# Optimization experiments

Measured on AMD Instinct MI355X. Metric: run time of the kernel, lower is better.

Reference implementation:

```python
import jax, jax.numpy as jnp
import numpy as np
from jax import lax

B, T, D, H = 64, 512, 512, 512


def setup_inputs() -> dict:
    key = jax.random.key(0)
    k1, k2, k3, k4 = jax.random.split(key, 4)
    inputs = jax.random.normal(k1, (B, T, D), dtype=jnp.float32)
    lengths = jax.random.randint(k2, (B,), 1, T + 1, dtype=jnp.int32)
    c0 = jnp.zeros((B, H), dtype=jnp.float32)
    h0 = jnp.zeros((B, H), dtype=jnp.float32)
    scale_i = 1.0 / np.sqrt(D)
    scale_h = 1.0 / np.sqrt(H)
    Wi = jax.random.normal(k3, (D, 4 * H), dtype=jnp.float32) * scale_i
    Wh = jax.random.normal(k4, (H, 4 * H), dtype=jnp.float32) * scale_h
    b = jnp.zeros((4 * H,), dtype=jnp.float32)
    return {"inputs": inputs, "lengths": lengths, "c0": c0, "h0": h0,
            "Wi": Wi, "Wh": Wh, "b": b, "reverse": 1}


def _flip_sequences(seq, lengths):
    # seq: [B, T, F]; keeps padding at the end while flipping valid prefix.
    t = seq.shape[1]
    idxs = (jnp.arange(t - 1, -1, -1)[None, :] + lengths[:, None]) % t  # [B, T]
    return jnp.take_along_axis(seq, idxs[:, :, None], axis=1)


def reference(inputs, lengths, c0, h0, Wi, Wh, b, reverse):
    batch, t, _ = inputs.shape
    if reverse:
        inputs = _flip_sequences(inputs, lengths)

    def step(carry, x_t):
        c, h = carry
        z = x_t @ Wi + h @ Wh + b  # [B, 4H]
        i_g, f_g, g_g, o_g = jnp.split(z, 4, axis=-1)
        c_new = jax.nn.sigmoid(f_g) * c + jax.nn.sigmoid(i_g) * jnp.tanh(g_g)
        h_new = jax.nn.sigmoid(o_g) * jnp.tanh(c_new)
        return (c_new, h_new), (c_new, h_new)

    xs = jnp.swapaxes(inputs, 0, 1)  # [T, B, D]
    _, (cs, hs) = lax.scan(step, (c0, h0), xs)
    cs = jnp.swapaxes(cs, 0, 1)  # [B, T, H]
    hs = jnp.swapaxes(hs, 0, 1)  # [B, T, H]
    outputs = hs

    last = lengths - 1
    bidx = jnp.arange(batch)
    c_final = cs[bidx, last]
    h_final = hs[bidx, last]

    if reverse:
        outputs = _flip_sequences(outputs, lengths)
    return outputs, (c_final, h_final)
```

## Files before the change

### kernel.cpp

```cpp
#include <hip/hip_runtime.h>

#define B_ 64
#define T_ 512
#define D_ 512
#define H_ 512
#define NG 2048

typedef __attribute__((ext_vector_type(8))) short short8;
typedef __attribute__((ext_vector_type(4))) float floatx4;
typedef __attribute__((ext_vector_type(4))) unsigned int uintx4;

static __device__ __forceinline__ unsigned short f2bf(float f) {
    unsigned int u = __float_as_uint(f);
    return (unsigned short)((u + 0x7FFFu + ((u >> 16) & 1u)) >> 16);
}

static __device__ __forceinline__ short8 pack8(float4 a, float4 b) {
    short8 r;
    r[0] = (short)f2bf(a.x); r[1] = (short)f2bf(a.y);
    r[2] = (short)f2bf(a.z); r[3] = (short)f2bf(a.w);
    r[4] = (short)f2bf(b.x); r[5] = (short)f2bf(b.y);
    r[6] = (short)f2bf(b.z); r[7] = (short)f2bf(b.w);
    return r;
}

static __device__ __forceinline__ float sigm(float x) { return 1.0f / (1.0f + __expf(-x)); }
static __device__ __forceinline__ float tanh_(float x) {
    float e = __expf(2.0f * x);
    return 1.0f - 2.0f / (e + 1.0f);
}

__global__ __launch_bounds__(256) void transpose_w(
    const float* __restrict__ Wi, const float* __restrict__ Wh,
    unsigned short* __restrict__ WiT, unsigned short* __restrict__ WhT)
{
    __shared__ float tile[64][65];
    const float* src = blockIdx.z ? Wh : Wi;
    unsigned short* dst = blockIdx.z ? WhT : WiT;
    const int n0 = blockIdx.x * 64, k0 = blockIdx.y * 64;
    const int cx = threadIdx.x & 63, ry = threadIdx.x >> 6;
#pragma unroll
    for (int i = 0; i < 16; ++i) {
        int k = ry * 16 + i;
        tile[k][cx] = src[(size_t)(k0 + k) * NG + n0 + cx];
    }
    __syncthreads();
#pragma unroll
    for (int i = 0; i < 16; ++i) {
        int n = ry * 16 + i;
        dst[(size_t)(n0 + n) * D_ + k0 + cx] = f2bf(tile[cx][n]);
    }
}

__global__ __launch_bounds__(256) void zx_gemm(
    const float* __restrict__ x, const int* __restrict__ lengths,
    const unsigned short* __restrict__ WiT, const float* __restrict__ bias,
    const int* __restrict__ revp, _Float16* __restrict__ zx)
{
    __shared__ unsigned short a_lds[128][40];
    __shared__ unsigned short b_lds[128][40];

    const int mt = blockIdx.x, nt = blockIdx.y;
    const int tid = threadIdx.x;
    const int lane = tid & 63, w = tid >> 6;
    const int wm = w & 1, wn = w >> 1;

    const int b = mt >> 2;
    const int len = lengths[b];
    const int rev = revp[0];

    const int r = tid >> 1;
    const int kh = (tid & 1) << 4;
    const int t = ((mt & 3) << 7) + r;
    const int src_t = rev ? ((T_ - 1 - t + len) & (T_ - 1)) : t;
    const float* arow = x + ((size_t)b * T_ + src_t) * D_;
    const unsigned short* brow = WiT + (size_t)(nt * 128 + r) * D_;

    floatx4 acc[4][4];
#pragma unroll
    for (int i = 0; i < 4; ++i)
#pragma unroll
        for (int j = 0; j < 4; ++j) acc[i][j] = (floatx4){0.f, 0.f, 0.f, 0.f};

    for (int kt = 0; kt < D_ / 32; ++kt) {
        const float4* ap = (const float4*)(arow + kt * 32 + kh);
        float4 a0 = ap[0], a1 = ap[1], a2 = ap[2], a3 = ap[3];
        const uint4* bp = (const uint4*)(brow + kt * 32 + kh);
        uint4 bq0 = bp[0], bq1 = bp[1];
        *(short8*)&a_lds[r][kh]     = pack8(a0, a1);
        *(short8*)&a_lds[r][kh + 8] = pack8(a2, a3);
        *(uint4*)&b_lds[r][kh]     = bq0;
        *(uint4*)&b_lds[r][kh + 8] = bq1;
        __syncthreads();

        short8 af[4], bfr[4];
#pragma unroll
        for (int mi = 0; mi < 4; ++mi)
            af[mi] = *(const short8*)&a_lds[wm * 64 + mi * 16 + (lane & 15)][(lane >> 4) << 3];
#pragma unroll
        for (int ni = 0; ni < 4; ++ni)
            bfr[ni] = *(const short8*)&b_lds[wn * 64 + ni * 16 + (lane & 15)][(lane >> 4) << 3];
#pragma unroll
        for (int mi = 0; mi < 4; ++mi)
#pragma unroll
            for (int ni = 0; ni < 4; ++ni)
                acc[mi][ni] = __builtin_amdgcn_mfma_f32_16x16x32_bf16(af[mi], bfr[ni], acc[mi][ni], 0, 0, 0);
        __syncthreads();
    }

#pragma unroll
    for (int mi = 0; mi < 4; ++mi) {
#pragma unroll
        for (int ni = 0; ni < 4; ++ni) {
            int row = wm * 64 + mi * 16 + ((lane >> 4) << 2);
            int col = nt * 128 + wn * 64 + ni * 16 + (lane & 15);
            float bv = bias[col];
            size_t base = (size_t)(mt * 128 + row) * NG + col;
#pragma unroll
            for (int v = 0; v < 4; ++v)
                zx[base + (size_t)v * NG] = (_Float16)(acc[mi][ni][v] + bv);
        }
    }
}

__global__ __launch_bounds__(256, 1) void lstm_rec(
    const _Float16* __restrict__ zx, const unsigned short* __restrict__ WhT,
    const float* __restrict__ c0, const float* __restrict__ h0,
    const int* __restrict__ lengths, const int* __restrict__ revp,
    float* __restrict__ out, unsigned int* __restrict__ hx)
{
    __shared__ unsigned short h_lds[16][520];
    __shared__ unsigned short h_next[16][32];

    const int bid = blockIdx.x;
    const int gb = bid & 3, gh = bid >> 2;
    const int tid = threadIdx.x;
    const int lane = tid & 63, w = tid >> 6;
    const int b0 = gb * 16, u0 = gh * 32;
    const int rev = revp[0];

    const int colh = lane & 15;
    const int rr = (lane >> 4) << 2;
    const int cg = colh >> 3;
    const int cu = colh & 7;
    const int uu = w * 8 + cu;
    const int khw = (lane >> 4) << 3;

    int len_v[4]; float c[4];
#pragma unroll
    for (int v = 0; v < 4; ++v) {
        len_v[v] = lengths[b0 + rr + v];
        c[v] = c0[(size_t)(b0 + rr + v) * H_ + u0 + uu];
    }

    short8 bw[16][2];
#pragma unroll
    for (int ni = 0; ni < 2; ++ni) {
        const unsigned short* src = WhT + (size_t)((ni * 2 + cg) * H_ + u0 + uu) * D_ + khw;
#pragma unroll
        for (int kk = 0; kk < 16; ++kk)
            bw[kk][ni] = *(const short8*)(src + kk * 32);
    }

    float zxv[2][4];
#pragma unroll
    for (int ni = 0; ni < 2; ++ni)
#pragma unroll
        for (int v = 0; v < 4; ++v)
            zxv[ni][v] = (float)zx[((size_t)(b0 + rr + v) * T_) * NG + (ni * 2 + cg) * H_ + u0 + uu];

    const int sr2 = tid & 15;
    const int ph  = tid >> 4;
    const int scc = ph * 32;
    const int probeq = (sr2 + ph) & 7;

    const int L = (w << 6) | lane;

    for (int s = 0; s < T_; ++s) {
        if (s == 0) {
            const float* hp = h0 + (size_t)(b0 + sr2) * H_ + scc;
#pragma unroll
            for (int q = 0; q < 4; ++q) {
                float4 f0 = *(const float4*)(hp + q * 8);
                float4 f1 = *(const float4*)(hp + q * 8 + 4);
                *(short8*)&h_lds[sr2][scc + q * 8] = pack8(f0, f1);
            }
        } else {
            const unsigned int* dp = hx + ((((unsigned)(s & 1) * 4 + gb) * 16 + ph) << 9) + (sr2 << 5);
            uintx4 k0, k1, k2, k3, k4, k5, k6, k7;
            for (;;) {
                asm volatile(
                    "global_load_dwordx4 %0, %8, off sc0 sc1\n\t"
                    "global_load_dwordx4 %1, %8, off offset:16 sc0 sc1\n\t"
                    "global_load_dwordx4 %2, %8, off offset:32 sc0 sc1\n\t"
                    "global_load_dwordx4 %3, %8, off offset:48 sc0 sc1\n\t"
                    "global_load_dwordx4 %4, %8, off offset:64 sc0 sc1\n\t"
                    "global_load_dwordx4 %5, %8, off offset:80 sc0 sc1\n\t"
                    "global_load_dwordx4 %6, %8, off offset:96 sc0 sc1\n\t"
                    "global_load_dwordx4 %7, %8, off offset:112 sc0 sc1\n\t"
                    "s_waitcnt vmcnt(0)"
                    : "=&v"(k0), "=&v"(k1), "=&v"(k2), "=&v"(k3),
                      "=&v"(k4), "=&v"(k5), "=&v"(k6), "=&v"(k7)
                    : "v"(dp) : "memory");
                const unsigned int tg = (unsigned int)s;
                bool ok = (k0[2] == tg) & (k1[2] == tg) & (k2[2] == tg) & (k3[2] == tg) &
                          (k4[2] == tg) & (k5[2] == tg) & (k6[2] == tg) & (k7[2] == tg);
                if (ok) break;
                const unsigned int* pp = dp + (probeq << 2) + 2;
                for (;;) {
                    unsigned int tv;
                    asm volatile("global_load_dword %0, %1, off sc0 sc1\n\t"
                                 "s_waitcnt vmcnt(0)"
                                 : "=v"(tv) : "v"(pp) : "memory");
                    if (tv == tg) break;
                    __builtin_amdgcn_s_sleep(1);
                }
            }
            uintx4 e;
            e[0] = k0[0]; e[1] = k0[1]; e[2] = k1[0]; e[3] = k1[1];
            *(uintx4*)&h_lds[sr2][scc]      = e;
            e[0] = k2[0]; e[1] = k2[1]; e[2] = k3[0]; e[3] = k3[1];
            *(uintx4*)&h_lds[sr2][scc + 8]  = e;
            e[0] = k4[0]; e[1] = k4[1]; e[2] = k5[0]; e[3] = k5[1];
            *(uintx4*)&h_lds[sr2][scc + 16] = e;
            e[0] = k6[0]; e[1] = k6[1]; e[2] = k7[0]; e[3] = k7[1];
            *(uintx4*)&h_lds[sr2][scc + 24] = e;
        }
        __syncthreads();

        floatx4 acc[2];
        acc[0] = (floatx4){0.f, 0.f, 0.f, 0.f};
        acc[1] = (floatx4){0.f, 0.f, 0.f, 0.f};
#pragma unroll
        for (int kk = 0; kk < 16; ++kk) {
            short8 af = *(const short8*)&h_lds[lane & 15][kk * 32 + khw];
            acc[0] = __builtin_amdgcn_mfma_f32_16x16x32_bf16(af, bw[kk][0], acc[0], 0, 0, 0);
            acc[1] = __builtin_amdgcn_mfma_f32_16x16x32_bf16(af, bw[kk][1], acc[1], 0, 0, 0);
        }

        float hn_v[4], cn_v[4];
#pragma unroll
        for (int v = 0; v < 4; ++v) {
            float own0 = acc[0][v] + zxv[0][v];
            float own1 = acc[1][v] + zxv[1][v];
            float oth0 = __shfl_xor(own0, 8);
            float oth1 = __shfl_xor(own1, 8);
            float zi = cg ? oth0 : own0;
            float zf = cg ? own0 : oth0;
            float zg = cg ? oth1 : own1;
            float zo = cg ? own1 : oth1;
            float ig = sigm(zi), fg = sigm(zf);
            float gg = tanh_(zg), og = sigm(zo);
            float cn = fg * c[v] + ig * gg;
            float hn = og * tanh_(cn);
            c[v] = cn; cn_v[v] = cn; hn_v[v] = hn;
            if (cg == 1)
                h_next[rr + v][uu] = f2bf(hn);
        }
        __syncthreads();

        if (L < 128 && s + 1 < T_) {
            const int pb = L >> 3, pu = (L & 7) << 2;
            uint2 hv = *(const uint2*)&h_next[pb][pu];
            uintx4 ck;
            ck[0] = hv.x; ck[1] = hv.y; ck[2] = (unsigned int)(s + 1); ck[3] = 0u;
            unsigned int* dst = hx + ((((unsigned)((s + 1) & 1) * 4 + gb) * 16 + gh) << 9) + (L << 2);
            asm volatile("global_store_dwordx4 %0, %1, off sc0 sc1"
                         :: "v"(dst), "v"(ck) : "memory");
        }

#pragma unroll
        for (int v = 0; v < 4; ++v) {
            const int b = b0 + rr + v;
            const int ug = u0 + uu;
            int orig_t = rev ? ((T_ - 1 - s + len_v[v]) & (T_ - 1)) : s;
            if (cg == 0)
                out[((size_t)b * T_ + orig_t) * H_ + ug] = hn_v[v];
            if (s == len_v[v] - 1) {
                size_t fin = (size_t)B_ * T_ * H_;
                if (cg == 0) out[fin + (size_t)b * H_ + ug] = cn_v[v];
                else         out[fin + (size_t)B_ * H_ + (size_t)b * H_ + ug] = hn_v[v];
            }
        }
        if (s + 1 < T_) {
#pragma unroll
            for (int ni = 0; ni < 2; ++ni)
#pragma unroll
                for (int v = 0; v < 4; ++v)
                    zxv[ni][v] = (float)zx[((size_t)(b0 + rr + v) * T_ + s + 1) * NG +
                                           (ni * 2 + cg) * H_ + u0 + uu];
        }
    }
}

extern "C" void kernel_launch(void* const* d_in, const int* in_sizes, int n_in,
                              void* d_out, int out_size, void* d_ws, size_t ws_size,
                              hipStream_t stream)
{
    const float* x       = (const float*)d_in[0];
    const int*   lengths = (const int*)d_in[1];
    const float* c0      = (const float*)d_in[2];
    const float* h0      = (const float*)d_in[3];
    const float* Wi      = (const float*)d_in[4];
    const float* Wh      = (const float*)d_in[5];
    const float* bias    = (const float*)d_in[6];
    const int*   revp    = (const int*)d_in[7];
    float* out = (float*)d_out;

    char* ws = (char*)d_ws;
    const size_t OFF_WIT = 0;
    const size_t OFF_WHT = 2ull << 20;
    const size_t OFF_ZX  = 4ull << 20;
    const size_t OFF_HX  = OFF_ZX + (size_t)B_ * T_ * NG * 2;
    const size_t HX_BYTES = 2ull * 4 * 16 * 128 * 16;
    const size_t NEED = OFF_HX + HX_BYTES;
    if (ws_size < NEED) return;

    unsigned short* WiT = (unsigned short*)(ws + OFF_WIT);
    unsigned short* WhT = (unsigned short*)(ws + OFF_WHT);
    _Float16* zx        = (_Float16*)(ws + OFF_ZX);
    unsigned int* hx    = (unsigned int*)(ws + OFF_HX);

    hipMemsetAsync(hx, 0, HX_BYTES, stream);
    dim3 gt(32, 8, 2);
    transpose_w<<<gt, 256, 0, stream>>>(Wi, Wh, WiT, WhT);
    dim3 g1(256, 16);
    zx_gemm<<<g1, 256, 0, stream>>>(x, lengths, WiT, bias, revp, zx);
    lstm_rec<<<64, 256, 0, stream>>>(zx, WhT, c0, h0, lengths, revp, out, hx);
}
```

Before: 1.888 ms.

## Publish h directly from registers and defer output stores to next step

```diff
diff --git a/kernel.cpp b/kernel.cpp
--- a/kernel.cpp
+++ b/kernel.cpp
@@ -130,7 +130,6 @@
     float* __restrict__ out, unsigned int* __restrict__ hx)
 {
     __shared__ unsigned short h_lds[16][520];
-    __shared__ unsigned short h_next[16][32];
 
     const int bid = blockIdx.x;
     const int gb = bid & 3, gh = bid >> 2;
@@ -169,25 +168,29 @@
         for (int v = 0; v < 4; ++v)
             zxv[ni][v] = (float)zx[((size_t)(b0 + rr + v) * T_) * NG + (ni * 2 + cg) * H_ + u0 + uu];
 
-    const int sr2 = tid & 15;
-    const int ph  = tid >> 4;
-    const int scc = ph * 32;
-    const int probeq = (sr2 + ph) & 7;
-
-    const int L = (w << 6) | lane;
+    const int q   = tid >> 6;
+    const int ph  = (tid >> 2) & 15;
+    const int o   = tid & 3;
+    const int crow = q * 4;
+    const int ccol = ph * 32 + o * 8;
+
+    float pend_hn[4], pend_cn[4];
+    int have_pend = 0, pend_s = 0;
 
     for (int s = 0; s < T_; ++s) {
         if (s == 0) {
-            const float* hp = h0 + (size_t)(b0 + sr2) * H_ + scc;
-#pragma unroll
-            for (int q = 0; q < 4; ++q) {
-                float4 f0 = *(const float4*)(hp + q * 8);
-                float4 f1 = *(const float4*)(hp + q * 8 + 4);
-                *(short8*)&h_lds[sr2][scc + q * 8] = pack8(f0, f1);
+            const float* hp = h0 + (size_t)(b0 + crow) * H_ + ccol;
+#pragma unroll
+            for (int v = 0; v < 4; ++v) {
+                float4 f0 = *(const float4*)(hp + (size_t)v * H_);
+                float4 f1 = *(const float4*)(hp + (size_t)v * H_ + 4);
+                *(short8*)&h_lds[crow + v][ccol] = pack8(f0, f1);
             }
         } else {
-            const unsigned int* dp = hx + ((((unsigned)(s & 1) * 4 + gb) * 16 + ph) << 9) + (sr2 << 5);
+            const unsigned int* dp =
+                hx + ((((unsigned)(s & 1) * 4 + gb) * 16 + ph) << 9) + ((q * 32 + o * 8) << 2);
             uintx4 k0, k1, k2, k3, k4, k5, k6, k7;
+            const unsigned int tg = (unsigned int)s;
             for (;;) {
                 asm volatile(
                     "global_load_dwordx4 %0, %8, off sc0 sc1\n\t"
@@ -202,29 +205,31 @@
                     : "=&v"(k0), "=&v"(k1), "=&v"(k2), "=&v"(k3),
                       "=&v"(k4), "=&v"(k5), "=&v"(k6), "=&v"(k7)
                     : "v"(dp) : "memory");
-                const unsigned int tg = (unsigned int)s;
                 bool ok = (k0[2] == tg) & (k1[2] == tg) & (k2[2] == tg) & (k3[2] == tg) &
                           (k4[2] == tg) & (k5[2] == tg) & (k6[2] == tg) & (k7[2] == tg);
                 if (ok) break;
-                const unsigned int* pp = dp + (probeq << 2) + 2;
-                for (;;) {
-                    unsigned int tv;
-                    asm volatile("global_load_dword %0, %1, off sc0 sc1\n\t"
-                                 "s_waitcnt vmcnt(0)"
-                                 : "=v"(tv) : "v"(pp) : "memory");
-                    if (tv == tg) break;
-                    __builtin_amdgcn_s_sleep(1);
-                }
             }
-            uintx4 e;
-            e[0] = k0[0]; e[1] = k0[1]; e[2] = k1[0]; e[3] = k1[1];
-            *(uintx4*)&h_lds[sr2][scc]      = e;
-            e[0] = k2[0]; e[1] = k2[1]; e[2] = k3[0]; e[3] = k3[1];
-            *(uintx4*)&h_lds[sr2][scc + 8]  = e;
-            e[0] = k4[0]; e[1] = k4[1]; e[2] = k5[0]; e[3] = k5[1];
-            *(uintx4*)&h_lds[sr2][scc + 16] = e;
-            e[0] = k6[0]; e[1] = k6[1]; e[2] = k7[0]; e[3] = k7[1];
-            *(uintx4*)&h_lds[sr2][scc + 24] = e;
+            uintx4 e0, e1, e2, e3;
+            e0[0] = (k0[0] & 0xffffu) | (k1[0] << 16);
+            e0[1] = (k2[0] & 0xffffu) | (k3[0] << 16);
+            e0[2] = (k4[0] & 0xffffu) | (k5[0] << 16);
+            e0[3] = (k6[0] & 0xffffu) | (k7[0] << 16);
+            e1[0] = (k0[0] >> 16) | (k1[0] & 0xffff0000u);
+            e1[1] = (k2[0] >> 16) | (k3[0] & 0xffff0000u);
+            e1[2] = (k4[0] >> 16) | (k5[0] & 0xffff0000u);
+            e1[3] = (k6[0] >> 16) | (k7[0] & 0xffff0000u);
+            e2[0] = (k0[1] & 0xffffu) | (k1[1] << 16);
+            e2[1] = (k2[1] & 0xffffu) | (k3[1] << 16);
+            e2[2] = (k4[1] & 0xffffu) | (k5[1] << 16);
+            e2[3] = (k6[1] & 0xffffu) | (k7[1] << 16);
+            e3[0] = (k0[1] >> 16) | (k1[1] & 0xffff0000u);
+            e3[1] = (k2[1] >> 16) | (k3[1] & 0xffff0000u);
+            e3[2] = (k4[1] >> 16) | (k5[1] & 0xffff0000u);
+            e3[3] = (k6[1] >> 16) | (k7[1] & 0xffff0000u);
+            *(uintx4*)&h_lds[crow + 0][ccol] = e0;
+            *(uintx4*)&h_lds[crow + 1][ccol] = e1;
+            *(uintx4*)&h_lds[crow + 2][ccol] = e2;
+            *(uintx4*)&h_lds[crow + 3][ccol] = e3;
         }
         __syncthreads();
 
@@ -237,8 +242,33 @@
             acc[0] = __builtin_amdgcn_mfma_f32_16x16x32_bf16(af, bw[kk][0], acc[0], 0, 0, 0);
             acc[1] = __builtin_amdgcn_mfma_f32_16x16x32_bf16(af, bw[kk][1], acc[1], 0, 0, 0);
         }
-
-        float hn_v[4], cn_v[4];
+        __syncthreads();
+
+        if (have_pend) {
+#pragma unroll
+            for (int v = 0; v < 4; ++v) {
+                const int b = b0 + rr + v;
+                const int ug = u0 + uu;
+                int orig_t = rev ? ((T_ - 1 - pend_s + len_v[v]) & (T_ - 1)) : pend_s;
+                if (cg == 0)
+                    out[((size_t)b * T_ + orig_t) * H_ + ug] = pend_hn[v];
+                if (pend_s == len_v[v] - 1) {
+                    size_t fin = (size_t)B_ * T_ * H_;
+                    if (cg == 0) out[fin + (size_t)b * H_ + ug] = pend_cn[v];
+                    else         out[fin + (size_t)B_ * H_ + (size_t)b * H_ + ug] = pend_hn[v];
+                }
+            }
+        }
+        float zxn[2][4];
+        if (s + 1 < T_) {
+#pragma unroll
+            for (int ni = 0; ni < 2; ++ni)
+#pragma unroll
+                for (int v = 0; v < 4; ++v)
+                    zxn[ni][v] = (float)zx[((size_t)(b0 + rr + v) * T_ + s + 1) * NG +
+                                           (ni * 2 + cg) * H_ + u0 + uu];
+        }
+
 #pragma unroll
         for (int v = 0; v < 4; ++v) {
             float own0 = acc[0][v] + zxv[0][v];
@@ -253,42 +283,40 @@
             float gg = tanh_(zg), og = sigm(zo);
             float cn = fg * c[v] + ig * gg;
             float hn = og * tanh_(cn);
-            c[v] = cn; cn_v[v] = cn; hn_v[v] = hn;
-            if (cg == 1)
-                h_next[rr + v][uu] = f2bf(hn);
-        }
-        __syncthreads();
-
-        if (L < 128 && s + 1 < T_) {
-            const int pb = L >> 3, pu = (L & 7) << 2;
-            uint2 hv = *(const uint2*)&h_next[pb][pu];
+            c[v] = cn; pend_cn[v] = cn; pend_hn[v] = hn;
+        }
+        pend_s = s; have_pend = 1;
+
+        if (cg == 1 && s + 1 < T_) {
             uintx4 ck;
-            ck[0] = hv.x; ck[1] = hv.y; ck[2] = (unsigned int)(s + 1); ck[3] = 0u;
-            unsigned int* dst = hx + ((((unsigned)((s + 1) & 1) * 4 + gb) * 16 + gh) << 9) + (L << 2);
+            ck[0] = (unsigned int)f2bf(pend_hn[0]) | ((unsigned int)f2bf(pend_hn[1]) << 16);
+            ck[1] = (unsigned int)f2bf(pend_hn[2]) | ((unsigned int)f2bf(pend_hn[3]) << 16);
+            ck[2] = (unsigned int)(s + 1); ck[3] = 0u;
+            unsigned int* dst = hx + ((((unsigned)((s + 1) & 1) * 4 + gb) * 16 + gh) << 9) +
+                                (((rr >> 2) * 32 + uu) << 2);
             asm volatile("global_store_dwordx4 %0, %1, off sc0 sc1"
                          :: "v"(dst), "v"(ck) : "memory");
         }
 
-#pragma unroll
-        for (int v = 0; v < 4; ++v) {
-            const int b = b0 + rr + v;
-            const int ug = u0 + uu;
-            int orig_t = rev ? ((T_ - 1 - s + len_v[v]) & (T_ - 1)) : s;
-            if (cg == 0)
-                out[((size_t)b * T_ + orig_t) * H_ + ug] = hn_v[v];
-            if (s == len_v[v] - 1) {
-                size_t fin = (size_t)B_ * T_ * H_;
-                if (cg == 0) out[fin + (size_t)b * H_ + ug] = cn_v[v];
-                else         out[fin + (size_t)B_ * H_ + (size_t)b * H_ + ug] = hn_v[v];
-            }
-        }
         if (s + 1 < T_) {
 #pragma unroll
             for (int ni = 0; ni < 2; ++ni)
 #pragma unroll
-                for (int v = 0; v < 4; ++v)
-                    zxv[ni][v] = (float)zx[((size_t)(b0 + rr + v) * T_ + s + 1) * NG +
-                                           (ni * 2 + cg) * H_ + u0 + uu];
+                for (int v = 0; v < 4; ++v) zxv[ni][v] = zxn[ni][v];
+        }
+    }
+
+#pragma unroll
+    for (int v = 0; v < 4; ++v) {
+        const int b = b0 + rr + v;
+        const int ug = u0 + uu;
+        int orig_t = rev ? ((T_ - 1 - pend_s + len_v[v]) & (T_ - 1)) : pend_s;
+        if (cg == 0)
+            out[((size_t)b * T_ + orig_t) * H_ + ug] = pend_hn[v];
+        if (pend_s == len_v[v] - 1) {
+            size_t fin = (size_t)B_ * T_ * H_;
+            if (cg == 0) out[fin + (size_t)b * H_ + ug] = pend_cn[v];
+            else         out[fin + (size_t)B_ * H_ + (size_t)b * H_ + ug] = pend_hn[v];
         }
     }
 }
```

Result: slower. 2.741 ms (+45.1%).

## Repartition LSTM recurrence blocks to 8 batch rows by 64 units with 512 threads

Applied to the files above, without the earlier changes.

```diff
diff --git a/kernel.cpp b/kernel.cpp
--- a/kernel.cpp
+++ b/kernel.cpp
@@ -123,34 +123,35 @@
     }
 }
 
-__global__ __launch_bounds__(256, 1) void lstm_rec(
+__global__ __launch_bounds__(512, 2) void lstm_rec(
     const _Float16* __restrict__ zx, const unsigned short* __restrict__ WhT,
     const float* __restrict__ c0, const float* __restrict__ h0,
     const int* __restrict__ lengths, const int* __restrict__ revp,
     float* __restrict__ out, unsigned int* __restrict__ hx)
 {
     __shared__ unsigned short h_lds[16][520];
-    __shared__ unsigned short h_next[16][32];
 
     const int bid = blockIdx.x;
-    const int gb = bid & 3, gh = bid >> 2;
+    const int gb = bid & 7, gh = bid >> 3;
     const int tid = threadIdx.x;
     const int lane = tid & 63, w = tid >> 6;
-    const int b0 = gb * 16, u0 = gh * 32;
+    const int b0 = gb * 8, u0 = gh * 64;
     const int rev = revp[0];
 
     const int colh = lane & 15;
     const int rr = (lane >> 4) << 2;
+    const int rb = rr & 7;
     const int cg = colh >> 3;
     const int cu = colh & 7;
     const int uu = w * 8 + cu;
     const int khw = (lane >> 4) << 3;
+    const bool rowok = (rr < 8);
 
     int len_v[4]; float c[4];
 #pragma unroll
     for (int v = 0; v < 4; ++v) {
-        len_v[v] = lengths[b0 + rr + v];
-        c[v] = c0[(size_t)(b0 + rr + v) * H_ + u0 + uu];
+        len_v[v] = lengths[b0 + rb + v];
+        c[v] = rowok ? c0[(size_t)(b0 + rr + v) * H_ + u0 + uu] : 0.0f;
     }
 
     short8 bw[16][2];
@@ -167,64 +168,79 @@
     for (int ni = 0; ni < 2; ++ni)
 #pragma unroll
         for (int v = 0; v < 4; ++v)
-            zxv[ni][v] = (float)zx[((size_t)(b0 + rr + v) * T_) * NG + (ni * 2 + cg) * H_ + u0 + uu];
-
-    const int sr2 = tid & 15;
-    const int ph  = tid >> 4;
-    const int scc = ph * 32;
-    const int probeq = (sr2 + ph) & 7;
-
-    const int L = (w << 6) | lane;
+            zxv[ni][v] = (float)zx[((size_t)(b0 + rb + v) * T_) * NG + (ni * 2 + cg) * H_ + u0 + uu];
+
+    for (int i = tid; i < 16 * 520; i += 512) ((unsigned short*)h_lds)[i] = 0;
+    __syncthreads();
 
     for (int s = 0; s < T_; ++s) {
-        if (s == 0) {
-            const float* hp = h0 + (size_t)(b0 + sr2) * H_ + scc;
-#pragma unroll
-            for (int q = 0; q < 4; ++q) {
-                float4 f0 = *(const float4*)(hp + q * 8);
-                float4 f1 = *(const float4*)(hp + q * 8 + 4);
-                *(short8*)&h_lds[sr2][scc + q * 8] = pack8(f0, f1);
-            }
-        } else {
-            const unsigned int* dp = hx + ((((unsigned)(s & 1) * 4 + gb) * 16 + ph) << 9) + (sr2 << 5);
-            uintx4 k0, k1, k2, k3, k4, k5, k6, k7;
-            for (;;) {
-                asm volatile(
-                    "global_load_dwordx4 %0, %8, off sc0 sc1\n\t"
-                    "global_load_dwordx4 %1, %8, off offset:16 sc0 sc1\n\t"
-                    "global_load_dwordx4 %2, %8, off offset:32 sc0 sc1\n\t"
-                    "global_load_dwordx4 %3, %8, off offset:48 sc0 sc1\n\t"
-                    "global_load_dwordx4 %4, %8, off offset:64 sc0 sc1\n\t"
-                    "global_load_dwordx4 %5, %8, off offset:80 sc0 sc1\n\t"
-                    "global_load_dwordx4 %6, %8, off offset:96 sc0 sc1\n\t"
-                    "global_load_dwordx4 %7, %8, off offset:112 sc0 sc1\n\t"
-                    "s_waitcnt vmcnt(0)"
-                    : "=&v"(k0), "=&v"(k1), "=&v"(k2), "=&v"(k3),
-                      "=&v"(k4), "=&v"(k5), "=&v"(k6), "=&v"(k7)
-                    : "v"(dp) : "memory");
+        if (w == 0) {
+            if (s == 0) {
+#pragma unroll
+                for (int b = 0; b < 8; ++b) {
+                    const float* hp = h0 + (size_t)(b0 + b) * H_ + lane * 8;
+                    float4 f0 = *(const float4*)hp;
+                    float4 f1 = *(const float4*)(hp + 4);
+                    *(short8*)&h_lds[b][lane * 8] = pack8(f0, f1);
+                }
+            } else {
                 const unsigned int tg = (unsigned int)s;
-                bool ok = (k0[2] == tg) & (k1[2] == tg) & (k2[2] == tg) & (k3[2] == tg) &
-                          (k4[2] == tg) & (k5[2] == tg) & (k6[2] == tg) & (k7[2] == tg);
-                if (ok) break;
-                const unsigned int* pp = dp + (probeq << 2) + 2;
+                const unsigned int grp = ((unsigned)(s & 1) * 8 + gb) * 1024;
+                const unsigned int* pp = hx + (size_t)(grp + (lane & 7) * 128 + 127) * 4 + 2;
                 for (;;) {
                     unsigned int tv;
                     asm volatile("global_load_dword %0, %1, off sc0 sc1\n\t"
                                  "s_waitcnt vmcnt(0)"
                                  : "=v"(tv) : "v"(pp) : "memory");
-                    if (tv == tg) break;
+                    if (__all(tv == tg)) break;
                     __builtin_amdgcn_s_sleep(1);
                 }
+#pragma unroll
+                for (int half = 0; half < 2; ++half) {
+                    const unsigned int* dp = hx + (size_t)(grp + lane * 16 + half * 8) * 4;
+                    uintx4 k0, k1, k2, k3, k4, k5, k6, k7;
+                    for (;;) {
+                        asm volatile(
+                            "global_load_dwordx4 %0, %8, off sc0 sc1\n\t"
+                            "global_load_dwordx4 %1, %8, off offset:16 sc0 sc1\n\t"
+                            "global_load_dwordx4 %2, %8, off offset:32 sc0 sc1\n\t"
+                            "global_load_dwordx4 %3, %8, off offset:48 sc0 sc1\n\t"
+                            "global_load_dwordx4 %4, %8, off offset:64 sc0 sc1\n\t"
+                            "global_load_dwordx4 %5, %8, off offset:80 sc0 sc1\n\t"
+                            "global_load_dwordx4 %6, %8, off offset:96 sc0 sc1\n\t"
+                            "global_load_dwordx4 %7, %8, off offset:112 sc0 sc1\n\t"
+                            "s_waitcnt vmcnt(0)"
+                            : "=&v"(k0), "=&v"(k1), "=&v"(k2), "=&v"(k3),
+                              "=&v"(k4), "=&v"(k5), "=&v"(k6), "=&v"(k7)
+                            : "v"(dp) : "memory");
+                        bool ok = (k0[2] == tg) & (k1[2] == tg) & (k2[2] == tg) & (k3[2] == tg) &
+                                  (k4[2] == tg) & (k5[2] == tg) & (k6[2] == tg) & (k7[2] == tg);
+                        if (ok) break;
+                        __builtin_amdgcn_s_sleep(1);
+                    }
+                    unsigned int pay[8][2];
+                    pay[0][0] = k0[0]; pay[0][1] = k0[1];
+                    pay[1][0] = k1[0]; pay[1][1] = k1[1];
+                    pay[2][0] = k2[0]; pay[2][1] = k2[1];
+                    pay[3][0] = k3[0]; pay[3][1] = k3[1];
+                    pay[4][0] = k4[0]; pay[4][1] = k4[1];
+                    pay[5][0] = k5[0]; pay[5][1] = k5[1];
+                    pay[6][0] = k6[0]; pay[6][1] = k6[1];
+                    pay[7][0] = k7[0]; pay[7][1] = k7[1];
+#pragma unroll
+                    for (int b = 0; b < 8; ++b) {
+                        const int q = b >> 2, hi = (b >> 1) & 1, sh = (b & 1) * 16;
+                        unsigned int x0 = (pay[0 * 2 + q][hi] >> sh) & 0xffffu;
+                        unsigned int x1 = (pay[1 * 2 + q][hi] >> sh) & 0xffffu;
+                        unsigned int x2 = (pay[2 * 2 + q][hi] >> sh) & 0xffffu;
+                        unsigned int x3 = (pay[3 * 2 + q][hi] >> sh) & 0xffffu;
+                        uint2 d;
+                        d.x = x0 | (x1 << 16);
+                        d.y = x2 | (x3 << 16);
+                        *(uint2*)&h_lds[b][lane * 8 + half * 4] = d;
+                    }
+                }
             }
-            uintx4 e;
-            e[0] = k0[0]; e[1] = k0[1]; e[2] = k1[0]; e[3] = k1[1];
-            *(uintx4*)&h_lds[sr2][scc]      = e;
-            e[0] = k2[0]; e[1] = k2[1]; e[2] = k3[0]; e[3] = k3[1];
-            *(uintx4*)&h_lds[sr2][scc + 8]  = e;
-            e[0] = k4[0]; e[1] = k4[1]; e[2] = k5[0]; e[3] = k5[1];
-            *(uintx4*)&h_lds[sr2][scc + 16] = e;
-            e[0] = k6[0]; e[1] = k6[1]; e[2] = k7[0]; e[3] = k7[1];
-            *(uintx4*)&h_lds[sr2][scc + 24] = e;
         }
         __syncthreads();
 
@@ -237,6 +253,7 @@
             acc[0] = __builtin_amdgcn_mfma_f32_16x16x32_bf16(af, bw[kk][0], acc[0], 0, 0, 0);
             acc[1] = __builtin_amdgcn_mfma_f32_16x16x32_bf16(af, bw[kk][1], acc[1], 0, 0, 0);
         }
+        __syncthreads();
 
         float hn_v[4], cn_v[4];
 #pragma unroll
@@ -254,32 +271,32 @@
             float cn = fg * c[v] + ig * gg;
             float hn = og * tanh_(cn);
             c[v] = cn; cn_v[v] = cn; hn_v[v] = hn;
-            if (cg == 1)
-                h_next[rr + v][uu] = f2bf(hn);
-        }
-        __syncthreads();
-
-        if (L < 128 && s + 1 < T_) {
-            const int pb = L >> 3, pu = (L & 7) << 2;
-            uint2 hv = *(const uint2*)&h_next[pb][pu];
+        }
+
+        if (cg == 1 && rowok && s + 1 < T_) {
             uintx4 ck;
-            ck[0] = hv.x; ck[1] = hv.y; ck[2] = (unsigned int)(s + 1); ck[3] = 0u;
-            unsigned int* dst = hx + ((((unsigned)((s + 1) & 1) * 4 + gb) * 16 + gh) << 9) + (L << 2);
+            ck[0] = (unsigned int)f2bf(hn_v[0]) | ((unsigned int)f2bf(hn_v[1]) << 16);
+            ck[1] = (unsigned int)f2bf(hn_v[2]) | ((unsigned int)f2bf(hn_v[3]) << 16);
+            ck[2] = (unsigned int)(s + 1); ck[3] = 0u;
+            unsigned int* dst = hx +
+                (size_t)((((unsigned)((s + 1) & 1) * 8 + gb) * 1024 + (u0 + uu) * 2 + (rr >> 2))) * 4;
             asm volatile("global_store_dwordx4 %0, %1, off sc0 sc1"
                          :: "v"(dst), "v"(ck) : "memory");
         }
 
-#pragma unroll
-        for (int v = 0; v < 4; ++v) {
-            const int b = b0 + rr + v;
-            const int ug = u0 + uu;
-            int orig_t = rev ? ((T_ - 1 - s + len_v[v]) & (T_ - 1)) : s;
-            if (cg == 0)
-                out[((size_t)b * T_ + orig_t) * H_ + ug] = hn_v[v];
-            if (s == len_v[v] - 1) {
-                size_t fin = (size_t)B_ * T_ * H_;
-                if (cg == 0) out[fin + (size_t)b * H_ + ug] = cn_v[v];
-                else         out[fin + (size_t)B_ * H_ + (size_t)b * H_ + ug] = hn_v[v];
+        if (rowok) {
+#pragma unroll
+            for (int v = 0; v < 4; ++v) {
+                const int b = b0 + rr + v;
+                const int ug = u0 + uu;
+                int orig_t = rev ? ((T_ - 1 - s + len_v[v]) & (T_ - 1)) : s;
+                if (cg == 0)
+                    out[((size_t)b * T_ + orig_t) * H_ + ug] = hn_v[v];
+                if (s == len_v[v] - 1) {
+                    size_t fin = (size_t)B_ * T_ * H_;
+                    if (cg == 0) out[fin + (size_t)b * H_ + ug] = cn_v[v];
+                    else         out[fin + (size_t)B_ * H_ + (size_t)b * H_ + ug] = hn_v[v];
+                }
             }
         }
         if (s + 1 < T_) {
@@ -287,7 +304,7 @@
             for (int ni = 0; ni < 2; ++ni)
 #pragma unroll
                 for (int v = 0; v < 4; ++v)
-                    zxv[ni][v] = (float)zx[((size_t)(b0 + rr + v) * T_ + s + 1) * NG +
+                    zxv[ni][v] = (float)zx[((size_t)(b0 + rb + v) * T_ + s + 1) * NG +
                                            (ni * 2 + cg) * H_ + u0 + uu];
         }
     }
@@ -312,7 +329,7 @@
     const size_t OFF_WHT = 2ull << 20;
     const size_t OFF_ZX  = 4ull << 20;
     const size_t OFF_HX  = OFF_ZX + (size_t)B_ * T_ * NG * 2;
-    const size_t HX_BYTES = 2ull * 4 * 16 * 128 * 16;
+    const size_t HX_BYTES = 2ull * 8 * 1024 * 16;
     const size_t NEED = OFF_HX + HX_BYTES;
     if (ws_size < NEED) return;
 
@@ -326,5 +343,5 @@
     transpose_w<<<gt, 256, 0, stream>>>(Wi, Wh, WiT, WhT);
     dim3 g1(256, 16);
     zx_gemm<<<g1, 256, 0, stream>>>(x, lengths, WiT, bias, revp, zx);
-    lstm_rec<<<64, 256, 0, stream>>>(zx, WhT, c0, h0, lengths, revp, out, hx);
-}
+    lstm_rec<<<64, 512, 0, stream>>>(zx, WhT, c0, h0, lengths, revp, out, hx);
+}
```

Measured after the change: 2.309 ms. +22.3%, slower.
